# Optimization experiments

Hardware: AMD Instinct MI355X
Metric: run time of the kernel (lower is better)

Reference implementation:

```python
import jax, jax.numpy as jnp
import numpy as np

MAX_ITERATIONS = 10
HALT_EPSILON = 0.01


def setup_inputs() -> dict:
    key = jax.random.key(0)
    ks = jax.random.split(key, 6)
    B, L, D, F = 4, 4096, 512, 2048
    state = jax.random.normal(ks[0], (B, L, D), jnp.float32)
    mask = jnp.ones((B, L), jnp.float32)
    # timestep signal added by ffn_preprocess(state, step)
    step_emb = jax.random.normal(ks[1], (MAX_ITERATIONS + 1, D), jnp.float32) * 0.02
    # pondering Dense(1, sigmoid, bias init 0.1)
    Wp = jax.random.normal(ks[2], (D, 1), jnp.float32) / np.sqrt(D)
    bp = jnp.full((1,), 0.1, jnp.float32)
    # position-wise FFN (ffn_transformation)
    W1 = jax.random.normal(ks[3], (D, F), jnp.float32) / np.sqrt(D)
    b1 = jnp.zeros((F,), jnp.float32)
    W2 = jax.random.normal(ks[4], (F, D), jnp.float32) / np.sqrt(F)
    b2 = jnp.zeros((D,), jnp.float32)
    return dict(state=state, mask=mask, step_emb=step_emb, Wp=Wp, bp=bp,
                W1=W1, b1=b1, W2=W2, b2=b2)


def _act(state, mask, step_emb, Wp, bp, W1, b1, W2, b2):
    threshold = 1.0 - HALT_EPSILON
    B, L, _ = state.shape
    hp = jnp.zeros((B, L), state.dtype)     # halting_probability
    rem = jnp.zeros((B, L), state.dtype)    # remainders
    nup = jnp.zeros((B, L), state.dtype)    # n_updates
    prev = jnp.zeros_like(state)            # previous_state (accumulator)

    def body(carry, t):
        st, hp, rem, nup, prev = carry
        # ffn_preprocess: add per-step timestep embedding
        s = st + step_emb[t][None, None, :]
        # pondering probability p: [B, L]
        p = jax.nn.sigmoid(jnp.einsum('bld,do->blo', s, Wp)[..., 0] + bp[0])
        still = (hp < 1.0).astype(st.dtype)
        q = hp + p * still
        new_halted = (q > threshold).astype(st.dtype) * still
        still = (q <= threshold).astype(st.dtype) * still
        hp = hp + p * still
        rem = rem + new_halted * (1.0 - hp)
        hp = hp + new_halted * rem
        nup = nup + still + new_halted
        uw = (p * still + new_halted * rem)[..., None]  # update_weights [B,L,1]
        # ffn_transformation: position-wise ReLU MLP, masked
        h = jnp.einsum('blf,fd->bld',
                       jax.nn.relu(jnp.einsum('bld,df->blf', s, W1) + b1), W2) + b2
        h = h * mask[..., None]
        # NOTE: original code overwrites the convex combination with a pure
        # accumulation: new_state = transformed * uw + previous_state
        new = h * uw + prev
        return (h, hp, rem, nup, new), None

    # Fixed-trip scan is math-equivalent to the tf.while_loop: once a position
    # halts, still/new_halted are 0 so hp/rem/nup/new_state are unchanged.
    (_, hp, rem, nup, prev), _ = jax.lax.scan(
        body, (state, hp, rem, nup, prev), jnp.arange(MAX_ITERATIONS + 1))
    return prev, nup, rem


def reference(state, mask, step_emb, Wp, bp, W1, b1, W2, b2):
    new_state, n_updates, remainders = _act(state, mask, step_emb, Wp, bp,
                                            W1, b1, W2, b2)
    return (new_state, (n_updates, remainders))
```

## Files before the change

kernel.cpp:

```cpp
#include <hip/hip_runtime.h>
#include <hip/hip_bf16.h>
#include <stdint.h>


#define THR 0.99f
typedef float4 f4;
typedef __attribute__((ext_vector_type(8))) short short8;
typedef __attribute__((ext_vector_type(4))) float f32x4;

__device__ __forceinline__ float ld_in(const void* p, long i, int bf) {
  if (bf) {
    unsigned short u = ((const unsigned short*)p)[i];
    return __uint_as_float(((unsigned int)u) << 16);
  }
  return ((const float*)p)[i];
}
__device__ __forceinline__ f4 ld4(const float* p) { return *(const f4*)p; }

__device__ __forceinline__ void split3(float x, unsigned short& h,
                                       unsigned short& m, unsigned short& l) {
  unsigned u = __float_as_uint(x);
  h = (unsigned short)(u >> 16);
  float fh = __uint_as_float(u & 0xFFFF0000u);
  float r = x - fh;
  unsigned v = __float_as_uint(r);
  m = (unsigned short)(v >> 16);
  float fm = __uint_as_float(v & 0xFFFF0000u);
  l = (unsigned short)(__float_as_uint(r - fm) >> 16);
}

__device__ __forceinline__ void gld16(const void* g, void* l) {
  __builtin_amdgcn_global_load_lds(
      (const __attribute__((address_space(1))) void*)g,
      (__attribute__((address_space(3))) void*)l, 16, 0, 0);
}

__global__ void k_detect(const void* mask, int* flag, const void* emb,
                         const void* Wp, const void* bp, const void* b1,
                         const void* b2, float* embF, float* WpF, float* bpF,
                         float* b1F, float* b2F) {
  __shared__ int sbf;
  if (threadIdx.x == 0) {
    unsigned int u = ((const unsigned int*)mask)[0];
    int bf = (u == 0x3F803F80u) ? 1 : 0;
    *flag = bf;
    sbf = bf;
  }
  __syncthreads();
  int bf = sbf;
  for (int i = threadIdx.x; i < 11 * 512; i += 256) embF[i] = ld_in(emb, i, bf);
  for (int i = threadIdx.x; i < 512; i += 256) WpF[i] = ld_in(Wp, i, bf);
  for (int i = threadIdx.x; i < 2048; i += 256) b1F[i] = ld_in(b1, i, bf);
  for (int i = threadIdx.x; i < 512; i += 256) b2F[i] = ld_in(b2, i, bf);
  if (threadIdx.x == 0) bpF[0] = ld_in(bp, 0, bf);
}

__global__ void k_init(const void* state, const void* W1, const void* W2,
                       const void* mask, const int* flag, float* stateF,
                       unsigned short* w1t, unsigned short* w2t, float* maskF,
                       float* prevF, float* hp, float* rem, float* nup,
                       int* counts) {
  int bf = *flag;
  long t = (long)blockIdx.x * blockDim.x + threadIdx.x;
  long st = (long)gridDim.x * blockDim.x;
  for (long i = t; i < 8388608L; i += st) {
    stateF[i] = ld_in(state, i, bf);
    prevF[i] = 0.f;
  }
  for (long i = t; i < 1048576L; i += st) {
    float v = ld_in(W1, i, bf);
    long n = i & 2047, k = i >> 11;
    unsigned short h, m, l;
    split3(v, h, m, l);
    long o = n * 512 + k;
    w1t[o] = h;
    w1t[1048576L + o] = m;
    w1t[2097152L + o] = l;
  }
  for (long i = t; i < 1048576L; i += st) {
    float v = ld_in(W2, i, bf);
    long k = i >> 9, n = i & 511;
    unsigned short h, m, l;
    split3(v, h, m, l);
    long o = n * 2048 + k;
    w2t[o] = h;
    w2t[1048576L + o] = m;
    w2t[2097152L + o] = l;
  }
  for (long i = t; i < 16384L; i += st) {
    maskF[i] = ld_in(mask, i, bf);
    hp[i] = 0.f;
    rem[i] = 0.f;
    nup[i] = 0.f;
  }
  if (t < 11) counts[t] = 0;
}

__global__ __launch_bounds__(256) void k_ponder(
    const float* __restrict__ stateF, const float* __restrict__ embF,
    const float* __restrict__ WpF, const float* __restrict__ bpF, float* hp,
    float* rem, float* nup, float* uw, int* __restrict__ count,
    int* __restrict__ ridx, int t) {
  int lane = threadIdx.x & 63;
  int pos = blockIdx.x * 4 + (threadIdx.x >> 6);
  float hpv = hp[pos];
  if (hpv >= 1.0f) return;
  const float* s = stateF + (long)pos * 512;
  const float* e = embF + t * 512;
  int d = lane * 8;
  f4 s0 = ld4(s + d), s1 = ld4(s + d + 4);
  f4 e0 = ld4(e + d), e1 = ld4(e + d + 4);
  f4 w0 = ld4(WpF + d), w1 = ld4(WpF + d + 4);
  float acc = (s0.x + e0.x) * w0.x;
  acc = fmaf(s0.y + e0.y, w0.y, acc);
  acc = fmaf(s0.z + e0.z, w0.z, acc);
  acc = fmaf(s0.w + e0.w, w0.w, acc);
  acc = fmaf(s1.x + e1.x, w1.x, acc);
  acc = fmaf(s1.y + e1.y, w1.y, acc);
  acc = fmaf(s1.z + e1.z, w1.z, acc);
  acc = fmaf(s1.w + e1.w, w1.w, acc);
#pragma unroll
  for (int off = 32; off > 0; off >>= 1) acc += __shfl_xor(acc, off, 64);
  if (lane == 0) {
    float p = 1.0f / (1.0f + expf(-(acc + bpF[0])));
    float q = hpv + p;
    float nh = (q > THR) ? 1.0f : 0.0f;
    float st2 = (q <= THR) ? 1.0f : 0.0f;
    float hpn = hpv + p * st2;
    float remn = rem[pos] + nh * (1.0f - hpn);
    hpn = hpn + nh * remn;
    nup[pos] = nup[pos] + st2 + nh;
    uw[pos] = p * st2 + nh * remn;
    hp[pos] = hpn;
    rem[pos] = remn;
    int idx = atomicAdd(count, 1);
    ridx[idx] = pos;
  }
}

#define MFMA16 __builtin_amdgcn_mfma_f32_16x16x32_bf16

#define PROD_LOOP()                                                            \
  _Pragma("unroll") for (int pb = 0; pb < 3; ++pb) {                           \
    short8 bfr[4];                                                             \
    _Pragma("unroll") for (int nt = 0; nt < 4; ++nt) bfr[nt] =                 \
        *(const short8*)&Bs[pb][quad][wn + nt * 16 + ln15][0];                 \
    int npa = (pb == 0) ? 3 : ((pb == 1) ? 2 : 1);                             \
    for (int pa = 0; pa < npa; ++pa)                                           \
      _Pragma("unroll") for (int mt = 0; mt < 4; ++mt)                         \
          _Pragma("unroll") for (int nt = 0; nt < 4; ++nt) acc[mt][nt] =       \
          MFMA16(af[pa][mt], bfr[nt], acc[mt][nt], 0, 0, 0);                   \
  }

#define BUILD_AF(DO_EMB)                                                       \
  short8 af[3][4];                                                             \
  _Pragma("unroll") for (int mt = 0; mt < 4; ++mt) {                           \
    int row = wm + mt * 16 + ln15;                                             \
    f4 x0 = *(const f4*)&Au[quad][0][row][0];                                  \
    f4 x1 = *(const f4*)&Au[quad][1][row][0];                                  \
    float xs[8];                                                               \
    xs[0] = x0.x; xs[1] = x0.y; xs[2] = x0.z; xs[3] = x0.w;                    \
    xs[4] = x1.x; xs[5] = x1.y; xs[6] = x1.z; xs[7] = x1.w;                    \
    if (DO_EMB) {                                                              \
      _Pragma("unroll") for (int j = 0; j < 8; ++j) xs[j] += es[j];            \
    }                                                                          \
    _Pragma("unroll") for (int j = 0; j < 8; ++j) {                            \
      unsigned short h, m, l;                                                  \
      split3(xs[j], h, m, l);                                                  \
      ((unsigned short*)&af[0][mt])[j] = h;                                    \
      ((unsigned short*)&af[1][mt])[j] = m;                                    \
      ((unsigned short*)&af[2][mt])[j] = l;                                    \
    }                                                                          \
  }

__global__ __launch_bounds__(256) void k_gemm1(
    const float* __restrict__ stateF, const float* __restrict__ embT,
    const unsigned short* __restrict__ w1t, const float* __restrict__ b1F,
    const int* __restrict__ count, const int* __restrict__ ridx,
    float* __restrict__ U, int c0, int mc) {
  int Ma = *count;
  int mEnd = c0 + mc;
  if (Ma < mEnd) mEnd = Ma;
  int f = blockIdx.x;
  int x = f & 7, s = f >> 3;
  int n0 = (x * 2 + (s & 1)) * 128;
  int m0 = c0 + (s >> 1) * 128;
  if (m0 >= mEnd) return;
  __shared__ __align__(16) float Au[4][2][128][4];
  __shared__ __align__(16) unsigned short Bs[3][4][128][8];
  __shared__ __align__(16) float embS[512];
  int tid = threadIdx.x;
  int lane = tid & 63, wv = tid >> 6;
  int quad = lane >> 4, ln15 = lane & 15;
  int wm = (wv >> 1) << 6, wn = (wv & 1) << 6;
  if (tid < 128) *(f4*)&embS[tid * 4] = ld4(embT + tid * 4);
  int rr0 = m0 + lane;
  if (rr0 >= mEnd) rr0 = mEnd - 1;
  int rr1 = m0 + 64 + lane;
  if (rr1 >= mEnd) rr1 = mEnd - 1;
  long pos0 = ridx[rr0], pos1 = ridx[rr1];
  f32x4 acc[4][4];
#pragma unroll
  for (int i = 0; i < 4; i++)
#pragma unroll
    for (int j = 0; j < 4; j++) acc[i][j] = (f32x4)0.f;
#pragma unroll 1
  for (int kt = 0; kt < 16; ++kt) {
    __syncthreads();
#pragma unroll
    for (int i = 0; i < 4; ++i) {
      int g = wv + 4 * i;
      int q = g >> 2, h = (g >> 1) & 1, rh = g & 1;
      long po = rh ? pos1 : pos0;
      gld16(stateF + po * 512 + kt * 32 + q * 8 + h * 4,
            &Au[q][h][rh * 64][0]);
    }
#pragma unroll
    for (int i = 0; i < 6; ++i) {
      int g = wv + 4 * i;
      int p = g >> 3, q = (g >> 1) & 3, rh = g & 1;
      long n = n0 + rh * 64 + lane;
      gld16(w1t + (long)p * 1048576L + n * 512 + kt * 32 + q * 8,
            &Bs[p][q][rh * 64][0]);
    }
    __syncthreads();
    float es[8];
    {
      f4 e0 = *(const f4*)&embS[kt * 32 + quad * 8];
      f4 e1 = *(const f4*)&embS[kt * 32 + quad * 8 + 4];
      es[0] = e0.x; es[1] = e0.y; es[2] = e0.z; es[3] = e0.w;
      es[4] = e1.x; es[5] = e1.y; es[6] = e1.z; es[7] = e1.w;
    }
    BUILD_AF(1);
    PROD_LOOP();
  }
#pragma unroll
  for (int mt = 0; mt < 4; ++mt)
#pragma unroll
    for (int reg = 0; reg < 4; ++reg) {
      int r = m0 + wm + mt * 16 + quad * 4 + reg;
      if (r < mEnd) {
        long lr = r - c0;
#pragma unroll
        for (int nt = 0; nt < 4; ++nt) {
          int n = n0 + wn + nt * 16 + ln15;
          U[lr * 2048 + n] = fmaxf(acc[mt][nt][reg] + b1F[n], 0.f);
        }
      }
    }
}

__global__ __launch_bounds__(256) void k_gemm2(
    const float* __restrict__ U, const unsigned short* __restrict__ w2t,
    const float* __restrict__ b2F, const int* __restrict__ count,
    const int* __restrict__ ridx, const float* __restrict__ maskF,
    const float* __restrict__ uwF, float* __restrict__ stateF,
    float* __restrict__ prevF, int c0, int mc) {
  int Ma = *count;
  int mEnd = c0 + mc;
  if (Ma < mEnd) mEnd = Ma;
  int f = blockIdx.x;
  int x = f & 7, s = f >> 3;
  int n0 = (x >> 1) * 128;
  int m0 = c0 + (s * 2 + (x & 1)) * 128;
  if (m0 >= mEnd) return;
  __shared__ __align__(16) float Au[4][2][128][4];
  __shared__ __align__(16) unsigned short Bs[3][4][128][8];
  int tid = threadIdx.x;
  int lane = tid & 63, wv = tid >> 6;
  int quad = lane >> 4, ln15 = lane & 15;
  int wm = (wv >> 1) << 6, wn = (wv & 1) << 6;
  long lr0 = (long)(m0 - c0) + lane;
  long lr1 = lr0 + 64;
  f32x4 acc[4][4];
#pragma unroll
  for (int i = 0; i < 4; i++)
#pragma unroll
    for (int j = 0; j < 4; j++) acc[i][j] = (f32x4)0.f;
#pragma unroll 1
  for (int kt = 0; kt < 64; ++kt) {
    __syncthreads();
#pragma unroll
    for (int i = 0; i < 4; ++i) {
      int g = wv + 4 * i;
      int q = g >> 2, h = (g >> 1) & 1, rh = g & 1;
      long lr = rh ? lr1 : lr0;
      gld16(U + lr * 2048 + kt * 32 + q * 8 + h * 4, &Au[q][h][rh * 64][0]);
    }
#pragma unroll
    for (int i = 0; i < 6; ++i) {
      int g = wv + 4 * i;
      int p = g >> 3, q = (g >> 1) & 3, rh = g & 1;
      long n = n0 + rh * 64 + lane;
      gld16(w2t + (long)p * 1048576L + n * 2048 + kt * 32 + q * 8,
            &Bs[p][q][rh * 64][0]);
    }
    __syncthreads();
    float es[8];
    (void)es;
    BUILD_AF(0);
    PROD_LOOP();
  }
#pragma unroll
  for (int mt = 0; mt < 4; ++mt)
#pragma unroll
    for (int reg = 0; reg < 4; ++reg) {
      int r = m0 + wm + mt * 16 + quad * 4 + reg;
      if (r < mEnd) {
        long pos = (long)ridx[r];
        float mk = maskF[pos];
        float uv = uwF[pos];
#pragma unroll
        for (int nt = 0; nt < 4; ++nt) {
          int n = n0 + wn + nt * 16 + ln15;
          float h = (acc[mt][nt][reg] + b2F[n]) * mk;
          long off = pos * 512 + n;
          stateF[off] = h;
          prevF[off] = fmaf(h, uv, prevF[off]);
        }
      }
    }
}

__global__ void k_final(const float* prevF, const float* nupF,
                        const float* remF, void* out, const int* flag) {
  long i = (long)blockIdx.x * 256 + threadIdx.x;
  if (i >= 8421376L) return;
  float v;
  if (i < 8388608L) v = prevF[i];
  else if (i < 8404992L) v = nupF[i - 8388608L];
  else v = remF[i - 8404992L];
  if (*flag) ((__hip_bfloat16*)out)[i] = __float2bfloat16(v);
  else ((float*)out)[i] = v;
}

extern "C" void kernel_launch(void* const* d_in, const int* in_sizes, int n_in,
                              void* d_out, int out_size, void* d_ws,
                              size_t ws_size, hipStream_t stream) {
  const void* state = d_in[0];
  const void* mask = d_in[1];
  const void* emb = d_in[2];
  const void* Wp = d_in[3];
  const void* bp = d_in[4];
  const void* W1 = d_in[5];
  const void* b1 = d_in[6];
  const void* W2 = d_in[7];
  const void* b2 = d_in[8];
  char* w = (char*)d_ws;
  float* stateF = (float*)(w + 0L);
  float* prevF = (float*)(w + 33554432L);
  unsigned short* w1t = (unsigned short*)(w + 67108864L);
  unsigned short* w2t = (unsigned short*)(w + 73400320L);
  float* maskF = (float*)(w + 79691776L);
  float* hp = (float*)(w + 79757312L);
  float* rem = (float*)(w + 79822848L);
  float* nup = (float*)(w + 79888384L);
  float* uwf = (float*)(w + 79953920L);
  float* embF = (float*)(w + 80019456L);
  float* WpF = (float*)(w + 80052224L);
  float* b1F = (float*)(w + 80056320L);
  float* b2F = (float*)(w + 80064512L);
  float* bpF = (float*)(w + 80068608L);
  int* flag = (int*)(w + 80068864L);
  int* counts = (int*)(w + 80069120L);
  int* ridx = (int*)(w + 80070144L);
  float* U = (float*)(w + 80791040L);
  long ub = (long)ws_size - 80791040L;
  long rows = ub / 8192L;
  long McL = rows & ~255L;
  if (McL > 16384L) McL = 16384L;
  if (McL < 256L) McL = 256L;
  int Mc = (int)McL;
  int nCh = (16384 + Mc - 1) / Mc;

  k_detect<<<1, 256, 0, stream>>>(mask, flag, emb, Wp, bp, b1, b2, embF, WpF,
                                  bpF, b1F, b2F);
  k_init<<<2048, 256, 0, stream>>>(state, W1, W2, mask, flag, stateF, w1t, w2t,
                                   maskF, prevF, hp, rem, nup, counts);
  for (int t = 0; t <= 10; t++) {
    k_ponder<<<4096, 256, 0, stream>>>(stateF, embF, WpF, bpF, hp, rem, nup,
                                       uwf, counts + t, ridx + (long)t * 16384,
                                       t);
    for (int c = 0; c < nCh; c++) {
      int c0 = c * Mc;
      int mc = 16384 - c0;
      if (mc > Mc) mc = Mc;
      int T = mc / 128;
      k_gemm1<<<T * 16, 256, 0, stream>>>(stateF, embF + t * 512, w1t, b1F,
                                          counts + t, ridx + (long)t * 16384,
                                          U, c0, mc);
      k_gemm2<<<T * 4, 256, 0, stream>>>(U, w2t, b2F, counts + t,
                                         ridx + (long)t * 16384, maskF, uwf,
                                         stateF, prevF, c0, mc);
    }
  }
  k_final<<<32896, 256, 0, stream>>>(prevF, nup, rem, d_out, flag);
}
```

Baseline: 1.992 ms.

## Double-buffer LDS tiles in both GEMM kernels to overlap loads with MFMA

Both GEMM kernels now use two LDS buffers, prefetching the next K-tile with direct global-to-LDS loads while the current tile is converted and multiplied. This halves the barriers per iteration and aims to hide global load latency behind MFMA work. The embedding staging buffer in LDS is removed and the embedding is read straight from global memory. LDS use roughly doubles, which may lower occupancy. Correctness depends on gld16 completing before the barrier, since there is no explicit vmcnt wait.

```diff
diff --git a/kernel.cpp b/kernel.cpp
--- a/kernel.cpp
+++ b/kernel.cpp
@@ -140,11 +140,11 @@
 
 #define MFMA16 __builtin_amdgcn_mfma_f32_16x16x32_bf16
 
-#define PROD_LOOP()                                                            \
+#define PROD_LOOP(BUF)                                                         \
   _Pragma("unroll") for (int pb = 0; pb < 3; ++pb) {                           \
     short8 bfr[4];                                                             \
     _Pragma("unroll") for (int nt = 0; nt < 4; ++nt) bfr[nt] =                 \
-        *(const short8*)&Bs[pb][quad][wn + nt * 16 + ln15][0];                 \
+        *(const short8*)&Bs[BUF][pb][quad][wn + nt * 16 + ln15][0];            \
     int npa = (pb == 0) ? 3 : ((pb == 1) ? 2 : 1);                             \
     for (int pa = 0; pa < npa; ++pa)                                           \
       _Pragma("unroll") for (int mt = 0; mt < 4; ++mt)                         \
@@ -152,12 +152,12 @@
           MFMA16(af[pa][mt], bfr[nt], acc[mt][nt], 0, 0, 0);                   \
   }
 
-#define BUILD_AF(DO_EMB)                                                       \
+#define BUILD_AF(BUF, DO_EMB)                                                  \
   short8 af[3][4];                                                             \
   _Pragma("unroll") for (int mt = 0; mt < 4; ++mt) {                           \
     int row = wm + mt * 16 + ln15;                                             \
-    f4 x0 = *(const f4*)&Au[quad][0][row][0];                                  \
-    f4 x1 = *(const f4*)&Au[quad][1][row][0];                                  \
+    f4 x0 = *(const f4*)&Au[BUF][quad][0][row][0];                             \
+    f4 x1 = *(const f4*)&Au[BUF][quad][1][row][0];                             \
     float xs[8];                                                               \
     xs[0] = x0.x; xs[1] = x0.y; xs[2] = x0.z; xs[3] = x0.w;                    \
     xs[4] = x1.x; xs[5] = x1.y; xs[6] = x1.z; xs[7] = x1.w;                    \
@@ -186,14 +186,12 @@
   int n0 = (x * 2 + (s & 1)) * 128;
   int m0 = c0 + (s >> 1) * 128;
   if (m0 >= mEnd) return;
-  __shared__ __align__(16) float Au[4][2][128][4];
-  __shared__ __align__(16) unsigned short Bs[3][4][128][8];
-  __shared__ __align__(16) float embS[512];
+  __shared__ __align__(16) float Au[2][4][2][128][4];
+  __shared__ __align__(16) unsigned short Bs[2][3][4][128][8];
   int tid = threadIdx.x;
   int lane = tid & 63, wv = tid >> 6;
   int quad = lane >> 4, ln15 = lane & 15;
   int wm = (wv >> 1) << 6, wn = (wv & 1) << 6;
-  if (tid < 128) *(f4*)&embS[tid * 4] = ld4(embT + tid * 4);
   int rr0 = m0 + lane;
   if (rr0 >= mEnd) rr0 = mEnd - 1;
   int rr1 = m0 + 64 + lane;
@@ -204,35 +202,41 @@
   for (int i = 0; i < 4; i++)
 #pragma unroll
     for (int j = 0; j < 4; j++) acc[i][j] = (f32x4)0.f;
+
+#define STAGE1(BUF, KT)                                                        \
+  {                                                                            \
+    _Pragma("unroll") for (int i = 0; i < 4; ++i) {                            \
+      int g = wv + 4 * i;                                                      \
+      int q = g >> 2, h = (g >> 1) & 1, rh = g & 1;                            \
+      long po = rh ? pos1 : pos0;                                              \
+      gld16(stateF + po * 512 + (KT) * 32 + q * 8 + h * 4,                     \
+            &Au[BUF][q][h][rh * 64][0]);                                       \
+    }                                                                          \
+    _Pragma("unroll") for (int i = 0; i < 6; ++i) {                            \
+      int g = wv + 4 * i;                                                      \
+      int p = g >> 3, q = (g >> 1) & 3, rh = g & 1;                            \
+      long n = n0 + rh * 64 + lane;                                            \
+      gld16(w1t + (long)p * 1048576L + n * 512 + (KT) * 32 + q * 8,           \
+            &Bs[BUF][p][q][rh * 64][0]);                                       \
+    }                                                                          \
+  }
+
+  STAGE1(0, 0);
+  __syncthreads();
 #pragma unroll 1
   for (int kt = 0; kt < 16; ++kt) {
-    __syncthreads();
-#pragma unroll
-    for (int i = 0; i < 4; ++i) {
-      int g = wv + 4 * i;
-      int q = g >> 2, h = (g >> 1) & 1, rh = g & 1;
-      long po = rh ? pos1 : pos0;
-      gld16(stateF + po * 512 + kt * 32 + q * 8 + h * 4,
-            &Au[q][h][rh * 64][0]);
-    }
-#pragma unroll
-    for (int i = 0; i < 6; ++i) {
-      int g = wv + 4 * i;
-      int p = g >> 3, q = (g >> 1) & 3, rh = g & 1;
-      long n = n0 + rh * 64 + lane;
-      gld16(w1t + (long)p * 1048576L + n * 512 + kt * 32 + q * 8,
-            &Bs[p][q][rh * 64][0]);
-    }
-    __syncthreads();
+    int cur = kt & 1;
+    if (kt + 1 < 16) STAGE1(cur ^ 1, kt + 1);
     float es[8];
     {
-      f4 e0 = *(const f4*)&embS[kt * 32 + quad * 8];
-      f4 e1 = *(const f4*)&embS[kt * 32 + quad * 8 + 4];
+      f4 e0 = ld4(embT + kt * 32 + quad * 8);
+      f4 e1 = ld4(embT + kt * 32 + quad * 8 + 4);
       es[0] = e0.x; es[1] = e0.y; es[2] = e0.z; es[3] = e0.w;
       es[4] = e1.x; es[5] = e1.y; es[6] = e1.z; es[7] = e1.w;
     }
-    BUILD_AF(1);
-    PROD_LOOP();
+    BUILD_AF(cur, 1);
+    PROD_LOOP(cur);
+    __syncthreads();
   }
 #pragma unroll
   for (int mt = 0; mt < 4; ++mt)
@@ -264,8 +268,8 @@
   int n0 = (x >> 1) * 128;
   int m0 = c0 + (s * 2 + (x & 1)) * 128;
   if (m0 >= mEnd) return;
-  __shared__ __align__(16) float Au[4][2][128][4];
-  __shared__ __align__(16) unsigned short Bs[3][4][128][8];
+  __shared__ __align__(16) float Au[2][4][2][128][4];
+  __shared__ __align__(16) unsigned short Bs[2][3][4][128][8];
   int tid = threadIdx.x;
   int lane = tid & 63, wv = tid >> 6;
   int quad = lane >> 4, ln15 = lane & 15;
@@ -277,29 +281,36 @@
   for (int i = 0; i < 4; i++)
 #pragma unroll
     for (int j = 0; j < 4; j++) acc[i][j] = (f32x4)0.f;
+
+#define STAGE2(BUF, KT)                                                        \
+  {                                                                            \
+    _Pragma("unroll") for (int i = 0; i < 4; ++i) {                            \
+      int g = wv + 4 * i;                                                      \
+      int q = g >> 2, h = (g >> 1) & 1, rh = g & 1;                            \
+      long lr = rh ? lr1 : lr0;                                                \
+      gld16(U + lr * 2048 + (KT) * 32 + q * 8 + h * 4,                         \
+            &Au[BUF][q][h][rh * 64][0]);                                       \
+    }                                                                          \
+    _Pragma("unroll") for (int i = 0; i < 6; ++i) {                            \
+      int g = wv + 4 * i;                                                      \
+      int p = g >> 3, q = (g >> 1) & 3, rh = g & 1;                            \
+      long n = n0 + rh * 64 + lane;                                            \
+      gld16(w2t + (long)p * 1048576L + n * 2048 + (KT) * 32 + q * 8,          \
+            &Bs[BUF][p][q][rh * 64][0]);                                       \
+    }                                                                          \
+  }
+
+  STAGE2(0, 0);
+  __syncthreads();
 #pragma unroll 1
   for (int kt = 0; kt < 64; ++kt) {
+    int cur = kt & 1;
+    if (kt + 1 < 64) STAGE2(cur ^ 1, kt + 1);
+    float es[8] = {0.f, 0.f, 0.f, 0.f, 0.f, 0.f, 0.f, 0.f};
+    (void)es;
+    BUILD_AF(cur, 0);
+    PROD_LOOP(cur);
     __syncthreads();
-#pragma unroll
-    for (int i = 0; i < 4; ++i) {
-      int g = wv + 4 * i;
-      int q = g >> 2, h = (g >> 1) & 1, rh = g & 1;
-      long lr = rh ? lr1 : lr0;
-      gld16(U + lr * 2048 + kt * 32 + q * 8 + h * 4, &Au[q][h][rh * 64][0]);
-    }
-#pragma unroll
-    for (int i = 0; i < 6; ++i) {
-      int g = wv + 4 * i;
-      int p = g >> 3, q = (g >> 1) & 3, rh = g & 1;
-      long n = n0 + rh * 64 + lane;
-      gld16(w2t + (long)p * 1048576L + n * 2048 + kt * 32 + q * 8,
-            &Bs[p][q][rh * 64][0]);
-    }
-    __syncthreads();
-    float es[8];
-    (void)es;
-    BUILD_AF(0);
-    PROD_LOOP();
   }
 #pragma unroll
   for (int mt = 0; mt < 4; ++mt)
```

Result: no change. 2.000 ms (+0.4%).

## Load A operands directly to registers with prefetch; double-buffer W2 tiles in gemm2

Applied to the files above, without the earlier changes.

Both GEMM kernels stop staging the activation (A) tile through shared memory. Each lane now loads its fragment straight into registers and prefetches the next k-step's fragment while the current one is split and multiplied. gemm2 also double-buffers the bf16 weight tiles in shared memory, so the next tile's global load overlaps the current MFMA work, and one of the two barriers per iteration goes away. In exchange, register pressure rises and LDS use in gemm2 doubles. gemm1's B staging is still single-buffered, and gemm1 now reads the embedding from global memory rather than LDS.

```diff
diff --git a/kernel.cpp b/kernel.cpp
--- a/kernel.cpp
+++ b/kernel.cpp
@@ -140,27 +140,14 @@
 
 #define MFMA16 __builtin_amdgcn_mfma_f32_16x16x32_bf16
 
-#define PROD_LOOP()                                                            \
-  _Pragma("unroll") for (int pb = 0; pb < 3; ++pb) {                           \
-    short8 bfr[4];                                                             \
-    _Pragma("unroll") for (int nt = 0; nt < 4; ++nt) bfr[nt] =                 \
-        *(const short8*)&Bs[pb][quad][wn + nt * 16 + ln15][0];                 \
-    int npa = (pb == 0) ? 3 : ((pb == 1) ? 2 : 1);                             \
-    for (int pa = 0; pa < npa; ++pa)                                           \
-      _Pragma("unroll") for (int mt = 0; mt < 4; ++mt)                         \
-          _Pragma("unroll") for (int nt = 0; nt < 4; ++nt) acc[mt][nt] =       \
-          MFMA16(af[pa][mt], bfr[nt], acc[mt][nt], 0, 0, 0);                   \
-  }
-
-#define BUILD_AF(DO_EMB)                                                       \
+#define BUILD_AF_REG(DO_EMB)                                                   \
   short8 af[3][4];                                                             \
   _Pragma("unroll") for (int mt = 0; mt < 4; ++mt) {                           \
-    int row = wm + mt * 16 + ln15;                                             \
-    f4 x0 = *(const f4*)&Au[quad][0][row][0];                                  \
-    f4 x1 = *(const f4*)&Au[quad][1][row][0];                                  \
     float xs[8];                                                               \
-    xs[0] = x0.x; xs[1] = x0.y; xs[2] = x0.z; xs[3] = x0.w;                    \
-    xs[4] = x1.x; xs[5] = x1.y; xs[6] = x1.z; xs[7] = x1.w;                    \
+    xs[0] = areg[mt][0].x; xs[1] = areg[mt][0].y;                              \
+    xs[2] = areg[mt][0].z; xs[3] = areg[mt][0].w;                              \
+    xs[4] = areg[mt][1].x; xs[5] = areg[mt][1].y;                              \
+    xs[6] = areg[mt][1].z; xs[7] = areg[mt][1].w;                              \
     if (DO_EMB) {                                                              \
       _Pragma("unroll") for (int j = 0; j < 8; ++j) xs[j] += es[j];            \
     }                                                                          \
@@ -171,6 +158,30 @@
       ((unsigned short*)&af[1][mt])[j] = m;                                    \
       ((unsigned short*)&af[2][mt])[j] = l;                                    \
     }                                                                          \
+  }
+
+#define PROD1()                                                                \
+  _Pragma("unroll") for (int pb = 0; pb < 3; ++pb) {                           \
+    short8 bfr[4];                                                             \
+    _Pragma("unroll") for (int nt = 0; nt < 4; ++nt) bfr[nt] =                 \
+        *(const short8*)&Bs[pb][quad][wn + nt * 16 + ln15][0];                 \
+    int npa = (pb == 0) ? 3 : ((pb == 1) ? 2 : 1);                             \
+    for (int pa = 0; pa < npa; ++pa)                                           \
+      _Pragma("unroll") for (int mt = 0; mt < 4; ++mt)                         \
+          _Pragma("unroll") for (int nt = 0; nt < 4; ++nt) acc[mt][nt] =       \
+          MFMA16(af[pa][mt], bfr[nt], acc[mt][nt], 0, 0, 0);                   \
+  }
+
+#define PROD2(BUF)                                                             \
+  _Pragma("unroll") for (int pb = 0; pb < 3; ++pb) {                           \
+    short8 bfr[4];                                                             \
+    _Pragma("unroll") for (int nt = 0; nt < 4; ++nt) bfr[nt] =                 \
+        *(const short8*)&Bs[BUF][pb][quad][wn + nt * 16 + ln15][0];            \
+    int npa = (pb == 0) ? 3 : ((pb == 1) ? 2 : 1);                             \
+    for (int pa = 0; pa < npa; ++pa)                                           \
+      _Pragma("unroll") for (int mt = 0; mt < 4; ++mt)                         \
+          _Pragma("unroll") for (int nt = 0; nt < 4; ++nt) acc[mt][nt] =       \
+          MFMA16(af[pa][mt], bfr[nt], acc[mt][nt], 0, 0, 0);                   \
   }
 
 __global__ __launch_bounds__(256) void k_gemm1(
@@ -186,53 +197,61 @@
   int n0 = (x * 2 + (s & 1)) * 128;
   int m0 = c0 + (s >> 1) * 128;
   if (m0 >= mEnd) return;
-  __shared__ __align__(16) float Au[4][2][128][4];
   __shared__ __align__(16) unsigned short Bs[3][4][128][8];
-  __shared__ __align__(16) float embS[512];
   int tid = threadIdx.x;
   int lane = tid & 63, wv = tid >> 6;
   int quad = lane >> 4, ln15 = lane & 15;
   int wm = (wv >> 1) << 6, wn = (wv & 1) << 6;
-  if (tid < 128) *(f4*)&embS[tid * 4] = ld4(embT + tid * 4);
-  int rr0 = m0 + lane;
-  if (rr0 >= mEnd) rr0 = mEnd - 1;
-  int rr1 = m0 + 64 + lane;
-  if (rr1 >= mEnd) rr1 = mEnd - 1;
-  long pos0 = ridx[rr0], pos1 = ridx[rr1];
+  long posA[4];
+#pragma unroll
+  for (int mt = 0; mt < 4; ++mt) {
+    int rA = m0 + wm + mt * 16 + ln15;
+    if (rA >= mEnd) rA = mEnd - 1;
+    posA[mt] = ridx[rA];
+  }
+  f4 areg[4][2];
+#pragma unroll
+  for (int mt = 0; mt < 4; ++mt) {
+    areg[mt][0] = ld4(stateF + posA[mt] * 512 + quad * 8);
+    areg[mt][1] = ld4(stateF + posA[mt] * 512 + quad * 8 + 4);
+  }
   f32x4 acc[4][4];
 #pragma unroll
   for (int i = 0; i < 4; i++)
 #pragma unroll
     for (int j = 0; j < 4; j++) acc[i][j] = (f32x4)0.f;
+
+#define STAGE_B1(KT)                                                           \
+  _Pragma("unroll") for (int i = 0; i < 6; ++i) {                              \
+    int g = wv + 4 * i;                                                        \
+    int p = g >> 3, q = (g >> 1) & 3, rh = g & 1;                              \
+    long n = n0 + rh * 64 + lane;                                              \
+    gld16(w1t + (long)p * 1048576L + n * 512 + (KT) * 32 + q * 8,             \
+          &Bs[p][q][rh * 64][0]);                                              \
+  }
+
 #pragma unroll 1
   for (int kt = 0; kt < 16; ++kt) {
     __syncthreads();
-#pragma unroll
-    for (int i = 0; i < 4; ++i) {
-      int g = wv + 4 * i;
-      int q = g >> 2, h = (g >> 1) & 1, rh = g & 1;
-      long po = rh ? pos1 : pos0;
-      gld16(stateF + po * 512 + kt * 32 + q * 8 + h * 4,
-            &Au[q][h][rh * 64][0]);
-    }
-#pragma unroll
-    for (int i = 0; i < 6; ++i) {
-      int g = wv + 4 * i;
-      int p = g >> 3, q = (g >> 1) & 3, rh = g & 1;
-      long n = n0 + rh * 64 + lane;
-      gld16(w1t + (long)p * 1048576L + n * 512 + kt * 32 + q * 8,
-            &Bs[p][q][rh * 64][0]);
-    }
-    __syncthreads();
+    STAGE_B1(kt);
     float es[8];
     {
-      f4 e0 = *(const f4*)&embS[kt * 32 + quad * 8];
-      f4 e1 = *(const f4*)&embS[kt * 32 + quad * 8 + 4];
+      f4 e0 = ld4(embT + kt * 32 + quad * 8);
+      f4 e1 = ld4(embT + kt * 32 + quad * 8 + 4);
       es[0] = e0.x; es[1] = e0.y; es[2] = e0.z; es[3] = e0.w;
       es[4] = e1.x; es[5] = e1.y; es[6] = e1.z; es[7] = e1.w;
     }
-    BUILD_AF(1);
-    PROD_LOOP();
+    BUILD_AF_REG(1);
+    if (kt + 1 < 16) {
+      int kg = (kt + 1) * 32 + quad * 8;
+#pragma unroll
+      for (int mt = 0; mt < 4; ++mt) {
+        areg[mt][0] = ld4(stateF + posA[mt] * 512 + kg);
+        areg[mt][1] = ld4(stateF + posA[mt] * 512 + kg + 4);
+      }
+    }
+    __syncthreads();
+    PROD1();
   }
 #pragma unroll
   for (int mt = 0; mt < 4; ++mt)
@@ -264,42 +283,55 @@
   int n0 = (x >> 1) * 128;
   int m0 = c0 + (s * 2 + (x & 1)) * 128;
   if (m0 >= mEnd) return;
-  __shared__ __align__(16) float Au[4][2][128][4];
-  __shared__ __align__(16) unsigned short Bs[3][4][128][8];
+  __shared__ __align__(16) unsigned short Bs[2][3][4][128][8];
   int tid = threadIdx.x;
   int lane = tid & 63, wv = tid >> 6;
   int quad = lane >> 4, ln15 = lane & 15;
   int wm = (wv >> 1) << 6, wn = (wv & 1) << 6;
-  long lr0 = (long)(m0 - c0) + lane;
-  long lr1 = lr0 + 64;
+  long rowA[4];
+#pragma unroll
+  for (int mt = 0; mt < 4; ++mt)
+    rowA[mt] = (long)(m0 - c0) + wm + mt * 16 + ln15;
+  f4 areg[4][2];
+#pragma unroll
+  for (int mt = 0; mt < 4; ++mt) {
+    areg[mt][0] = ld4(U + rowA[mt] * 2048 + quad * 8);
+    areg[mt][1] = ld4(U + rowA[mt] * 2048 + quad * 8 + 4);
+  }
   f32x4 acc[4][4];
 #pragma unroll
   for (int i = 0; i < 4; i++)
 #pragma unroll
     for (int j = 0; j < 4; j++) acc[i][j] = (f32x4)0.f;
+
+#define STAGE_B2(BUF, KT)                                                      \
+  _Pragma("unroll") for (int i = 0; i < 6; ++i) {                              \
+    int g = wv + 4 * i;                                                        \
+    int p = g >> 3, q = (g >> 1) & 3, rh = g & 1;                              \
+    long n = n0 + rh * 64 + lane;                                              \
+    gld16(w2t + (long)p * 1048576L + n * 2048 + (KT) * 32 + q * 8,            \
+          &Bs[BUF][p][q][rh * 64][0]);                                         \
+  }
+
+  STAGE_B2(0, 0);
+  __syncthreads();
 #pragma unroll 1
   for (int kt = 0; kt < 64; ++kt) {
+    int cur = kt & 1;
+    if (kt + 1 < 64) STAGE_B2(cur ^ 1, kt + 1);
+    float es[8] = {0.f, 0.f, 0.f, 0.f, 0.f, 0.f, 0.f, 0.f};
+    (void)es;
+    BUILD_AF_REG(0);
+    if (kt + 1 < 64) {
+      int kg = (kt + 1) * 32 + quad * 8;
+#pragma unroll
+      for (int mt = 0; mt < 4; ++mt) {
+        areg[mt][0] = ld4(U + rowA[mt] * 2048 + kg);
+        areg[mt][1] = ld4(U + rowA[mt] * 2048 + kg + 4);
+      }
+    }
+    PROD2(cur);
     __syncthreads();
-#pragma unroll
-    for (int i = 0; i < 4; ++i) {
-      int g = wv + 4 * i;
-      int q = g >> 2, h = (g >> 1) & 1, rh = g & 1;
-      long lr = rh ? lr1 : lr0;
-      gld16(U + lr * 2048 + kt * 32 + q * 8 + h * 4, &Au[q][h][rh * 64][0]);
-    }
-#pragma unroll
-    for (int i = 0; i < 6; ++i) {
-      int g = wv + 4 * i;
-      int p = g >> 3, q = (g >> 1) & 3, rh = g & 1;
-      long n = n0 + rh * 64 + lane;
-      gld16(w2t + (long)p * 1048576L + n * 2048 + kt * 32 + q * 8,
-            &Bs[p][q][rh * 64][0]);
-    }
-    __syncthreads();
-    float es[8];
-    (void)es;
-    BUILD_AF(0);
-    PROD_LOOP();
   }
 #pragma unroll
   for (int mt = 0; mt < 4; ++mt)
```

After: 2.134 ms. 1.07x slower.
